# Kernel tuning notes

Measured on AMD Instinct MI355X. Metric: run time of the kernel, lower is better.

## Reference

```python
import jax, jax.numpy as jnp
import numpy as np

# Constants from the torch module __init__
FACE_INDS = np.array([[0, 1, 2, 3], [0, 4, 2, 6], [0, 1, 4, 5],
                      [1, 3, 5, 7], [2, 3, 6, 7], [4, 5, 6, 7]])  # (6,4)
N_GRID = 11
N_POINTS = N_GRID * N_GRID        # 121
N_FACE = 6
N_KP_HAND = 21
N_CONTACTS = 10
ITA = 0.2
IND1 = np.array([0, 1, 2, 3])
IND2 = np.array([1, 2, 3, 0])


def _bilinear_grid():
    # grid[p, k] = bilinear weights for the 4 face corners, p over 11x11 (u,v)
    g = []
    for u in np.linspace(0.0, 1.0, N_GRID):
        for v in np.linspace(0.0, 1.0, N_GRID):
            g.append([v * (1 - u), v * u, (1 - v) * (1 - u), u * (1 - v)])
    return jnp.asarray(np.array(g, dtype=np.float32))  # (121, 4)


def setup_inputs() -> dict:
    key = jax.random.key(0)
    poses = jax.random.normal(key, (8192, N_KP_HAND + 8, 3), dtype=jnp.float32)
    return {"poses": poses}


def affinity_loss(poses):
    bs = poses.shape[0]
    hand = poses[:, :N_KP_HAND, :]          # (bs, 21, 3)
    obj = poses[:, N_KP_HAND:, :]           # (bs, 8, 3)

    # --- sample_face_points: bilinear sample 121 pts on each of the 6 faces ---
    grid = _bilinear_grid().astype(poses.dtype)        # (121, 4)
    faces = obj[:, FACE_INDS, :]                        # (bs, 6, 4, 3)
    face_points = jnp.einsum('bfkc,pk->bfpc', faces, grid)  # (bs, 6, 121, 3)
    obj_pts = face_points.reshape(bs, N_FACE * N_POINTS, 3)  # (bs, 726, 3)

    xx = jnp.sum(hand * hand, axis=-1)                  # (bs, 21)
    yy = jnp.sum(obj_pts * obj_pts, axis=-1)            # (bs, 726)
    zz = jnp.einsum('bic,bjc->bij', hand, obj_pts)      # (bs, 21, 726)
    pdist = jnp.sqrt(xx[:, :, None] + yy[:, None, :] - 2.0 * zz + 1e-6)
    pdist = pdist.reshape(bs, N_KP_HAND, N_FACE, N_POINTS)

    # --- per (hand kp, face) nearest face point, then global top-10 contacts ---
    dist_h2f = jnp.min(pdist, axis=3)                   # (bs, 21, 6)
    idxs_h2f = jnp.argmin(pdist, axis=3)                # (bs, 21, 6)
    flat = dist_h2f.reshape(bs, N_KP_HAND * N_FACE)     # (bs, 126)
    order = jnp.argsort(flat, axis=1)[:, :N_CONTACTS]   # (bs, 10)
    dist = jnp.take_along_axis(flat, order, axis=1)     # (bs, 10)
    inds_hand = order // N_FACE
    inds_face = order % N_FACE
    b = jnp.arange(bs)[:, None]
    ind_obj = idxs_h2f[b, inds_hand, inds_face]                     # (bs, 10)
    obj_contacts = obj_pts[b, inds_face * N_POINTS + ind_obj]       # (bs, 10, 3)

    # --- get_obj_info: axis endpoints and mean edge length of the bbox ---
    points1 = obj[:, :4, :].mean(axis=1)                # (bs, 3)
    points2 = obj[:, 4:, :].mean(axis=1)                # (bs, 3)
    l1 = jnp.linalg.norm(obj[:, IND1] - obj[:, IND2], axis=-1).mean(1, keepdims=True)
    l2 = jnp.linalg.norm(obj[:, IND1 + 4] - obj[:, IND2 + 4], axis=-1).mean(1, keepdims=True)
    length = (l1 + l2) * 0.5                            # (bs, 1)

    mask1 = (dist < length * ITA).astype(poses.dtype)   # (bs, 10)
    mask = mask1[:, :, None] * mask1[:, None, :]        # (bs, 10, 10)

    direct_vec = points2 - points1                      # (bs, 3)
    dv_norm = jnp.linalg.norm(direct_vec, axis=1, keepdims=True)  # (bs, 1)
    normed_dv = direct_vec / (dv_norm + 1e-5)
    vec_contacts = obj_contacts - points1[:, None, :]   # (bs, 10, 3)
    inner = jnp.sum(direct_vec[:, None, :] * vec_contacts, axis=-1)  # (bs, 10)
    t = inner / (dv_norm + 1e-5)                        # (bs, 10)
    r = points1[:, None, :] + normed_dv[:, None, :] * t[:, :, None]  # (bs, 10, 3)
    normal_vec = obj_contacts - r
    normal_vec = normal_vec / (jnp.linalg.norm(normal_vec, axis=2, keepdims=True) + 1e-5)
    cos_sim = jnp.einsum('bic,bjc->bij', normal_vec, normal_vec)  # (bs, 10, 10)

    return (cos_sim * mask).sum() / (mask.sum() + 1.0)


def reference(poses):
    return affinity_loss(poses)
```

## Files before the change

### kernel.cpp

```cpp
#include <hip/hip_runtime.h>
#include <math.h>

#define NGRID   11
#define NPAIR   126
#define NCONT   10

#define NSUB    64
#define NBUK    128
#define WS_SUB  16
#define WS_BUK  128
#define WS_WORDS (WS_BUK + 2 * NBUK)

#define NBUCKET 256

typedef float v2f __attribute__((ext_vector_type(2)));
#define FMA2(a,b,c) __builtin_elementwise_fma((a),(b),(c))
#define MAX2(a,b)   __builtin_elementwise_max((a),(b))
#define SP2(x)      ((v2f){(x),(x)})

__device__ __forceinline__ int last_hit(unsigned old, unsigned quota) {
    const unsigned r = old + 1u - quota;
    return (r == 0u) || (r == 0xAAAAAAAAu);
}

__device__ __constant__ int4 c_face4[6] = {
    {0,1,2,3},{0,4,2,6},{0,1,4,5},{1,3,5,7},{2,3,6,7},{4,5,6,7}};
__device__ __constant__ float c_U[NGRID] = {
    0.0f,0.1f,0.2f,0.3f,0.4f,0.5f,0.6f,0.7f,0.8f,0.9f,1.0f};

__global__ void zero_ws_kernel(float* ws, int n) {
    int t = blockIdx.x * 256 + threadIdx.x;
    if (t < n) ws[t] = 0.0f;
}

__device__ __forceinline__ void coefs_from_face(
        const float4* __restrict__ Ff, float hx, float hy, float hz,
        float& C00, float& C10, float& C01, float& C11,
        float& C20, float& C02, float& C21, float& C12, float& C22) {
    const float4 F0 = Ff[0], F1 = Ff[1], F2 = Ff[2],
                 F3 = Ff[3], F4 = Ff[4], F5 = Ff[5];
    const float hx2 = 2.0f * hx, hy2 = 2.0f * hy, hz2 = 2.0f * hz;
    const float ha2 = fmaf(hx2, F0.x, fmaf(hy2, F0.y, hz2 * F0.z));
    const float hb2 = fmaf(hx2, F1.x, fmaf(hy2, F1.y, hz2 * F1.z));
    const float hc2 = fmaf(hx2, F2.x, fmaf(hy2, F2.y, hz2 * F2.z));
    const float hd2 = fmaf(hx2, F3.x, fmaf(hy2, F3.y, hz2 * F3.z));
    C00 = ha2 - F0.w;
    C10 = hb2 - F4.x;
    C01 = hc2 - F4.y;
    C11 = hd2 - F4.z;
    C20 = -F1.w;  C02 = -F2.w;  C21 = -F4.w;  C12 = -F5.x;  C22 = -F3.w;
}

__launch_bounds__(256)
__global__ void affinity_kernel(const float* __restrict__ poses,
                                float* __restrict__ ws,
                                float* __restrict__ out,
                                int bs, int mode) {
    const int t    = threadIdx.x;
    const int half = t >> 7;
    const int t0   = t & 127;
    const int batch = blockIdx.x * 2 + half;
    const bool valid = batch < bs;

    __shared__ float    sh_pose[2][88];
    __shared__ float4   sh_face[2][36];
    __shared__ float    sh_thr[2][2];
    __shared__ int      sh_ru[2][128];
    __shared__ int      sh_cpair[2][128];
    __shared__ unsigned sh_cnt[2], sh_cnt2[2];
    __shared__ unsigned sh_key[2][128];
    __shared__ float    sh_cont[2][128][3];
    __shared__ float    sh_win[2][NCONT][3];
    __shared__ float    sh_nd[2][2];
    __shared__ int      sh_last;
    __shared__ double   sh_rn[4], sh_rd[4];

    if (valid && t0 < 87) sh_pose[half][t0] = poses[(size_t)batch * 87 + t0];
    if (t0 == 127) { sh_cnt[half] = 0u; sh_cnt2[half] = 0u; }
    __syncthreads();

    const float* hand = sh_pose[half];
    const float* obj  = sh_pose[half] + 63;

    if (valid && t0 < 6) {
        const int4 F = c_face4[t0];
        float C0[3], C1[3], C2[3], C3[3];
        #pragma unroll
        for (int c = 0; c < 3; ++c) {
            C0[c] = obj[F.x * 3 + c];
            C1[c] = obj[F.y * 3 + c];
            C2[c] = obj[F.z * 3 + c];
            C3[c] = obj[F.w * 3 + c];
        }
        float av[3], bv[3], cv[3], dv[3];
        #pragma unroll
        for (int c = 0; c < 3; ++c) {
            av[c] = C2[c];
            bv[c] = C3[c] - C2[c];
            cv[c] = C0[c] - C2[c];
            dv[c] = C1[c] - C0[c] - C3[c] + C2[c];
        }
        float aa=0.f,bb=0.f,cc=0.f,dd=0.f,ab=0.f,ac=0.f,ad=0.f,bc=0.f,bd=0.f,cd=0.f;
        #pragma unroll
        for (int c = 0; c < 3; ++c) {
            aa += av[c]*av[c]; bb += bv[c]*bv[c];
            cc += cv[c]*cv[c]; dd += dv[c]*dv[c];
            ab += av[c]*bv[c]; ac += av[c]*cv[c];
            ad += av[c]*dv[c]; bc += bv[c]*cv[c];
            bd += bv[c]*dv[c]; cd += cv[c]*dv[c];
        }
        float4* Ff = &sh_face[half][t0 * 6];
        Ff[0] = make_float4(av[0], av[1], av[2], aa);
        Ff[1] = make_float4(bv[0], bv[1], bv[2], bb);
        Ff[2] = make_float4(cv[0], cv[1], cv[2], cc);
        Ff[3] = make_float4(dv[0], dv[1], dv[2], dd);
        Ff[4] = make_float4(2.f*ab, 2.f*ac, 2.f*(ad+bc), 2.f*bd);
        Ff[5] = make_float4(2.f*cd, 0.f, 0.f, 0.f);
    }
    if (valid && t0 == 6) {
        float l1 = 0.0f, l2 = 0.0f;
        #pragma unroll
        for (int e = 0; e < 4; ++e) {
            const int a = e, b2 = (e + 1) & 3;
            {
                const float dx = obj[a*3+0]-obj[b2*3+0];
                const float dy = obj[a*3+1]-obj[b2*3+1];
                const float dz = obj[a*3+2]-obj[b2*3+2];
                l1 += sqrtf(dx*dx + dy*dy + dz*dz);
            }
            {
                const float dx = obj[(a+4)*3+0]-obj[(b2+4)*3+0];
                const float dy = obj[(a+4)*3+1]-obj[(b2+4)*3+1];
                const float dz = obj[(a+4)*3+2]-obj[(b2+4)*3+2];
                l2 += sqrtf(dx*dx + dy*dy + dz*dz);
            }
        }
        l1 *= 0.25f; l2 *= 0.25f;
        const float L02 = (l1 + l2) * 0.5f * 0.2f;
        sh_thr[half][0] = L02 * L02 - 1e-6f + 1e-2f;
        sh_thr[half][1] = L02;
    }
    __syncthreads();

    if (valid && t0 < NPAIR) {
        const int i = t0 / 6;
        const int f = t0 - i * 6;
        const float hx = hand[i*3+0], hy = hand[i*3+1], hz = hand[i*3+2];
        const float xx = hx*hx + hy*hy + hz*hz;
        float C00,C10,C01,C11,C20,C02,C21,C12,C22;
        coefs_from_face(&sh_face[half][f*6], hx, hy, hz,
                        C00,C10,C01,C11,C20,C02,C21,C12,C22);

        const float U[NGRID] = {0.0f,0.1f,0.2f,0.3f,0.4f,0.5f,
                                0.6f,0.7f,0.8f,0.9f,1.0f};
        float qb = -3.0e38f;
        int   ru = 0;
        #pragma unroll
        for (int rp = 0; rp < 5; ++rp) {
            const v2f u2 = (v2f){U[2*rp], U[2*rp+1]};
            const v2f A2 = FMA2(FMA2(SP2(C22), u2, SP2(C12)), u2, SP2(C02));
            const v2f A1 = FMA2(FMA2(SP2(C21), u2, SP2(C11)), u2, SP2(C01));
            const v2f A0 = FMA2(FMA2(SP2(C20), u2, SP2(C10)), u2, SP2(C00));
            v2f m2 = A0;
            #pragma unroll
            for (int iv = 1; iv < NGRID; ++iv) {
                const v2f vv = SP2(U[iv]);
                m2 = MAX2(m2, FMA2(FMA2(A2, vv, A1), vv, A0));
            }
            if (m2.x > qb) { qb = m2.x; ru = 2*rp; }
            if (m2.y > qb) { qb = m2.y; ru = 2*rp + 1; }
        }
        {
            const float u = 1.0f;
            const float A2 = fmaf(fmaf(C22,u,C12),u,C02);
            const float A1 = fmaf(fmaf(C21,u,C11),u,C01);
            const float A0 = fmaf(fmaf(C20,u,C10),u,C00);
            float m1 = A0;
            #pragma unroll
            for (int iv = 1; iv < NGRID; ++iv)
                m1 = fmaxf(m1, fmaf(fmaf(A2,U[iv],A1),U[iv],A0));
            if (m1 > qb) { qb = m1; ru = 10; }
        }
        sh_ru[half][t0] = ru;
        const float d2s = xx - qb;
        if (d2s < sh_thr[half][0]) {
            const unsigned s = atomicAdd(&sh_cnt[half], 1u);
            sh_cpair[half][s] = t0;
        }
    }
    __syncthreads();

    {
        const int cnt = (int)sh_cnt[half];
        if (t0 < cnt) {
            const int pair = sh_cpair[half][t0];
            const int i  = pair / 6;
            const int f  = pair - 6 * i;
            const int ru = sh_ru[half][pair];
            const float hx = hand[i*3+0], hy = hand[i*3+1], hz = hand[i*3+2];
            float C00,C10,C01,C11,C20,C02,C21,C12,C22;
            coefs_from_face(&sh_face[half][f*6], hx, hy, hz,
                            C00,C10,C01,C11,C20,C02,C21,C12,C22);
            const float u  = c_U[ru];
            const float A2 = fmaf(fmaf(C22,u,C12),u,C02);
            const float A1 = fmaf(fmaf(C21,u,C11),u,C01);
            const float A0 = fmaf(fmaf(C20,u,C10),u,C00);
            const float U[NGRID] = {0.0f,0.1f,0.2f,0.3f,0.4f,0.5f,
                                    0.6f,0.7f,0.8f,0.9f,1.0f};
            float qr = A0; int vb = 0;
            #pragma unroll
            for (int iv = 1; iv < NGRID; ++iv) {
                const float q = fmaf(fmaf(A2,U[iv],A1),U[iv],A0);
                if (q > qr) { qr = q; vb = iv; }
            }
            const double du = ru * 0.1;
            const double dv = vb * 0.1;
            const float w0 = (float)(dv * (1.0 - du));
            const float w1 = (float)(dv * du);
            const float w2 = (float)((1.0 - dv) * (1.0 - du));
            const float w3 = (float)(du * (1.0 - dv));
            const int4 F = c_face4[f];
            const int i0 = F.x*3, i1 = F.y*3, i2 = F.z*3, i3 = F.w*3;
            const float cx = w0*obj[i0+0]+w1*obj[i1+0]+w2*obj[i2+0]+w3*obj[i3+0];
            const float cy = w0*obj[i0+1]+w1*obj[i1+1]+w2*obj[i2+1]+w3*obj[i3+1];
            const float cz = w0*obj[i0+2]+w1*obj[i1+2]+w2*obj[i2+2]+w3*obj[i3+2];
            const float xx = hx*hx + hy*hy + hz*hz;
            const float yy = cx*cx + cy*cy + cz*cz;
            const float zz = hx*cx + hy*cy + hz*cz;
            const float d2e = (xx + yy) - 2.0f * zz;
            const float dist = sqrtf(d2e + 1e-6f);
            if (dist < sh_thr[half][1]) {
                const unsigned s2 = atomicAdd(&sh_cnt2[half], 1u);
                const float d2k = fmaxf(d2e, 0.0f);
                sh_key[half][s2] = (__float_as_uint(d2k) & 0xFFFFFF80u)
                                 | (unsigned)pair;
                sh_cont[half][s2][0] = cx;
                sh_cont[half][s2][1] = cy;
                sh_cont[half][s2][2] = cz;
            }
        }
    }
    __syncthreads();

    const int n2 = (int)sh_cnt2[half];
    if (t0 < n2) {
        const unsigned ke = sh_key[half][t0];
        int rank = 0;
        for (int j = 0; j < n2; ++j) rank += (sh_key[half][j] < ke) ? 1 : 0;
        if (rank < NCONT) {
            sh_win[half][rank][0] = sh_cont[half][t0][0];
            sh_win[half][rank][1] = sh_cont[half][t0][1];
            sh_win[half][rank][2] = sh_cont[half][t0][2];
        }
    }
    __syncthreads();

    const int kwin = n2 < NCONT ? n2 : NCONT;
    float px = 0.f, py = 0.f, pz = 0.f;
    if (valid && t0 < kwin) {
        const float cx = sh_win[half][t0][0];
        const float cy = sh_win[half][t0][1];
        const float cz = sh_win[half][t0][2];
        const float p1x = (((obj[0] +obj[3]) +obj[6]) +obj[9]) *0.25f;
        const float p1y = (((obj[1] +obj[4]) +obj[7]) +obj[10])*0.25f;
        const float p1z = (((obj[2] +obj[5]) +obj[8]) +obj[11])*0.25f;
        const float p2x = (((obj[12]+obj[15])+obj[18])+obj[21])*0.25f;
        const float p2y = (((obj[13]+obj[16])+obj[19])+obj[22])*0.25f;
        const float p2z = (((obj[14]+obj[17])+obj[20])+obj[23])*0.25f;
        const float dvx = p2x-p1x, dvy = p2y-p1y, dvz = p2z-p1z;
        const float dvn = sqrtf(dvx*dvx + dvy*dvy + dvz*dvz);
        const float den = dvn + 1e-5f;
        const float ndx = dvx/den, ndy = dvy/den, ndz = dvz/den;
        const float vcx = cx-p1x, vcy = cy-p1y, vcz = cz-p1z;
        const float inner = dvx*vcx + dvy*vcy + dvz*vcz;
        const float tp = inner / den;
        const float rx = p1x + ndx*tp, ry = p1y + ndy*tp, rz = p1z + ndz*tp;
        float nvx = cx-rx, nvy = cy-ry, nvz = cz-rz;
        const float nvn = sqrtf(nvx*nvx + nvy*nvy + nvz*nvz) + 1e-5f;
        px = nvx / nvn; py = nvy / nvn; pz = nvz / nvn;
    }
    if (t0 < 64) {
        #pragma unroll
        for (int off = 32; off >= 1; off >>= 1) {
            px += __shfl_xor(px, off, 64);
            py += __shfl_xor(py, off, 64);
            pz += __shfl_xor(pz, off, 64);
        }
        if (t0 == 0) {
            sh_nd[half][0] = px*px + py*py + pz*pz;
            sh_nd[half][1] = (float)(kwin * kwin);
        }
    }
    __syncthreads();

    if (t == 0) {
        sh_last = 0;
        const float num = sh_nd[0][0] + sh_nd[1][0];
        const float dnm = sh_nd[0][1] + sh_nd[1][1];
        const int b = blockIdx.x;
        if (mode) {
            float* bkt = ws + WS_BUK + 2 * (b & (NBUK - 1));
            const float r0 = atomicAdd(bkt + 0, num);
            const float r1 = atomicAdd(bkt + 1, dnm);
            asm volatile("" :: "v"(r0), "v"(r1) : "memory");
            unsigned* subs = (unsigned*)ws + WS_SUB;
            const unsigned nb = gridDim.x;
            const unsigned g  = (unsigned)b & (NSUB - 1);
            const unsigned quota = (nb - 1u - g) / NSUB + 1u;
            const unsigned old = atomicAdd(subs + g, 1u);
            if (last_hit(old, quota)) {
                const unsigned ngroups = nb < NSUB ? nb : NSUB;
                const unsigned m2 = atomicAdd((unsigned*)ws, 1u);
                if (last_hit(m2, ngroups)) sh_last = 1;
            }
        } else {
            float* bucket = ws + 2 * (b & (NBUCKET - 1));
            atomicAdd(bucket + 0, num);
            atomicAdd(bucket + 1, dnm);
        }
    }
    __syncthreads();

    if (sh_last) {
        double n = 0.0, d = 0.0;
        if (t < NBUK) {
            float* bkt = ws + WS_BUK + 2 * t;
            n = (double)atomicAdd(bkt + 0, 0.0f);
            d = (double)atomicAdd(bkt + 1, 0.0f);
        }
        #pragma unroll
        for (int off = 32; off >= 1; off >>= 1) {
            n += __shfl_xor(n, off, 64);
            d += __shfl_xor(d, off, 64);
        }
        const int w = t >> 6;
        if ((t & 63) == 0) { sh_rn[w] = n; sh_rd[w] = d; }
        __syncthreads();
        if (t == 0) {
            const double nn = sh_rn[0] + sh_rn[1] + sh_rn[2] + sh_rn[3];
            const double dd = sh_rd[0] + sh_rd[1] + sh_rd[2] + sh_rd[3];
            out[0] = (float)(nn / (dd + 1.0));
        }
    }
}

__launch_bounds__(1024)
__global__ void finalize_kernel(const float* __restrict__ ws,
                                float* __restrict__ out, int nslot) {
    const int t = threadIdx.x;
    __shared__ double sh_n[16], sh_d[16];
    double n = 0.0, d = 0.0;
    for (int k = t; k < nslot; k += 1024) {
        n += (double)ws[2 * k + 0];
        d += (double)ws[2 * k + 1];
    }
    #pragma unroll
    for (int off = 32; off >= 1; off >>= 1) {
        n += __shfl_xor(n, off, 64);
        d += __shfl_xor(d, off, 64);
    }
    const int w = t >> 6;
    if ((t & 63) == 0) { sh_n[w] = n; sh_d[w] = d; }
    __syncthreads();
    if (t == 0) {
        double nn = 0.0, dd = 0.0;
        #pragma unroll
        for (int i = 0; i < 16; ++i) { nn += sh_n[i]; dd += sh_d[i]; }
        out[0] = (float)(nn / (dd + 1.0));
    }
}

extern "C" void kernel_launch(void* const* d_in, const int* in_sizes, int n_in,
                              void* d_out, int out_size, void* d_ws, size_t ws_size,
                              hipStream_t stream) {
    const float* poses = (const float*)d_in[0];
    float* out = (float*)d_out;
    float* ws  = (float*)d_ws;
    const int bs = in_sizes[0] / 87;
    const int nblk = (bs + 1) / 2;

    if (ws_size >= (size_t)WS_WORDS * sizeof(float)) {
        hipLaunchKernelGGL(affinity_kernel, dim3(nblk), dim3(256), 0, stream,
                           poses, ws, out, bs, 1);
    } else {
        hipLaunchKernelGGL(zero_ws_kernel, dim3(1), dim3(256), 0, stream,
                           ws, NBUCKET * 2);
        hipLaunchKernelGGL(affinity_kernel, dim3(nblk), dim3(256), 0, stream,
                           poses, ws, out, bs, 0);
        hipLaunchKernelGGL(finalize_kernel, dim3(1), dim3(1024), 0, stream,
                           ws, out, NBUCKET);
    }
}
```

Measured before the change: 76.13 us.

## Map one batch element per wavefront and replace block barriers with ballot compaction

Each 64-lane wavefront now handles one batch element, so a block covers four elements instead of two. Lanes loop over the 126 hand-face pairs in two passes and compute face coefficients inline rather than staging them in shared memory. Candidate compaction uses ballot/popcount instead of LDS atomics, and wave barriers replace most __syncthreads. This cuts block-wide syncs and atomics and halves the grid, at the cost of serialising pairs per lane, some redundant face-coefficient math, and a looped rank sort.

```diff
diff --git a/kernel.cpp b/kernel.cpp
--- a/kernel.cpp
+++ b/kernel.cpp
@@ -31,24 +31,6 @@
 __global__ void zero_ws_kernel(float* ws, int n) {
     int t = blockIdx.x * 256 + threadIdx.x;
     if (t < n) ws[t] = 0.0f;
-}
-
-__device__ __forceinline__ void coefs_from_face(
-        const float4* __restrict__ Ff, float hx, float hy, float hz,
-        float& C00, float& C10, float& C01, float& C11,
-        float& C20, float& C02, float& C21, float& C12, float& C22) {
-    const float4 F0 = Ff[0], F1 = Ff[1], F2 = Ff[2],
-                 F3 = Ff[3], F4 = Ff[4], F5 = Ff[5];
-    const float hx2 = 2.0f * hx, hy2 = 2.0f * hy, hz2 = 2.0f * hz;
-    const float ha2 = fmaf(hx2, F0.x, fmaf(hy2, F0.y, hz2 * F0.z));
-    const float hb2 = fmaf(hx2, F1.x, fmaf(hy2, F1.y, hz2 * F1.z));
-    const float hc2 = fmaf(hx2, F2.x, fmaf(hy2, F2.y, hz2 * F2.z));
-    const float hd2 = fmaf(hx2, F3.x, fmaf(hy2, F3.y, hz2 * F3.z));
-    C00 = ha2 - F0.w;
-    C10 = hb2 - F4.x;
-    C01 = hc2 - F4.y;
-    C11 = hd2 - F4.z;
-    C20 = -F1.w;  C02 = -F2.w;  C21 = -F4.w;  C12 = -F5.x;  C22 = -F3.w;
 }
 
 __launch_bounds__(256)
@@ -57,67 +39,34 @@
                                 float* __restrict__ out,
                                 int bs, int mode) {
     const int t    = threadIdx.x;
-    const int half = t >> 7;
-    const int t0   = t & 127;
-    const int batch = blockIdx.x * 2 + half;
+    const int w    = t >> 6;
+    const int lane = t & 63;
+    const int batch = blockIdx.x * 4 + w;
     const bool valid = batch < bs;
 
-    __shared__ float    sh_pose[2][88];
-    __shared__ float4   sh_face[2][36];
-    __shared__ float    sh_thr[2][2];
-    __shared__ int      sh_ru[2][128];
-    __shared__ int      sh_cpair[2][128];
-    __shared__ unsigned sh_cnt[2], sh_cnt2[2];
-    __shared__ unsigned sh_key[2][128];
-    __shared__ float    sh_cont[2][128][3];
-    __shared__ float    sh_win[2][NCONT][3];
-    __shared__ float    sh_nd[2][2];
+    __shared__ float    sh_pose[352];
+    __shared__ unsigned sh_key[4][128];
+    __shared__ float    sh_cont[4][128][3];
+    __shared__ float    sh_win[4][NCONT][3];
+    __shared__ float    sh_nd[4][2];
     __shared__ int      sh_last;
     __shared__ double   sh_rn[4], sh_rd[4];
 
-    if (valid && t0 < 87) sh_pose[half][t0] = poses[(size_t)batch * 87 + t0];
-    if (t0 == 127) { sh_cnt[half] = 0u; sh_cnt2[half] = 0u; }
+    {
+        const size_t lim = (size_t)bs * 87;
+        const size_t g0  = (size_t)blockIdx.x * 348 + t;
+        if (t < 348 && g0 < lim) sh_pose[t] = poses[g0];
+        const int t2 = t + 256;
+        const size_t g1 = g0 + 256;
+        if (t2 < 348 && g1 < lim) sh_pose[t2] = poses[g1];
+    }
     __syncthreads();
 
-    const float* hand = sh_pose[half];
-    const float* obj  = sh_pose[half] + 63;
-
-    if (valid && t0 < 6) {
-        const int4 F = c_face4[t0];
-        float C0[3], C1[3], C2[3], C3[3];
-        #pragma unroll
-        for (int c = 0; c < 3; ++c) {
-            C0[c] = obj[F.x * 3 + c];
-            C1[c] = obj[F.y * 3 + c];
-            C2[c] = obj[F.z * 3 + c];
-            C3[c] = obj[F.w * 3 + c];
-        }
-        float av[3], bv[3], cv[3], dv[3];
-        #pragma unroll
-        for (int c = 0; c < 3; ++c) {
-            av[c] = C2[c];
-            bv[c] = C3[c] - C2[c];
-            cv[c] = C0[c] - C2[c];
-            dv[c] = C1[c] - C0[c] - C3[c] + C2[c];
-        }
-        float aa=0.f,bb=0.f,cc=0.f,dd=0.f,ab=0.f,ac=0.f,ad=0.f,bc=0.f,bd=0.f,cd=0.f;
-        #pragma unroll
-        for (int c = 0; c < 3; ++c) {
-            aa += av[c]*av[c]; bb += bv[c]*bv[c];
-            cc += cv[c]*cv[c]; dd += dv[c]*dv[c];
-            ab += av[c]*bv[c]; ac += av[c]*cv[c];
-            ad += av[c]*dv[c]; bc += bv[c]*cv[c];
-            bd += bv[c]*dv[c]; cd += cv[c]*dv[c];
-        }
-        float4* Ff = &sh_face[half][t0 * 6];
-        Ff[0] = make_float4(av[0], av[1], av[2], aa);
-        Ff[1] = make_float4(bv[0], bv[1], bv[2], bb);
-        Ff[2] = make_float4(cv[0], cv[1], cv[2], cc);
-        Ff[3] = make_float4(dv[0], dv[1], dv[2], dd);
-        Ff[4] = make_float4(2.f*ab, 2.f*ac, 2.f*(ad+bc), 2.f*bd);
-        Ff[5] = make_float4(2.f*cd, 0.f, 0.f, 0.f);
-    }
-    if (valid && t0 == 6) {
+    const float* hand = sh_pose + w * 87;
+    const float* obj  = hand + 63;
+
+    float L02 = 0.0f, flagthr = -3.0e38f;
+    if (valid) {
         float l1 = 0.0f, l2 = 0.0f;
         #pragma unroll
         for (int e = 0; e < 4; ++e) {
@@ -136,131 +85,158 @@
             }
         }
         l1 *= 0.25f; l2 *= 0.25f;
-        const float L02 = (l1 + l2) * 0.5f * 0.2f;
-        sh_thr[half][0] = L02 * L02 - 1e-6f + 1e-2f;
-        sh_thr[half][1] = L02;
-    }
-    __syncthreads();
-
-    if (valid && t0 < NPAIR) {
-        const int i = t0 / 6;
-        const int f = t0 - i * 6;
-        const float hx = hand[i*3+0], hy = hand[i*3+1], hz = hand[i*3+2];
-        const float xx = hx*hx + hy*hy + hz*hz;
-        float C00,C10,C01,C11,C20,C02,C21,C12,C22;
-        coefs_from_face(&sh_face[half][f*6], hx, hy, hz,
-                        C00,C10,C01,C11,C20,C02,C21,C12,C22);
-
-        const float U[NGRID] = {0.0f,0.1f,0.2f,0.3f,0.4f,0.5f,
-                                0.6f,0.7f,0.8f,0.9f,1.0f};
-        float qb = -3.0e38f;
-        int   ru = 0;
-        #pragma unroll
-        for (int rp = 0; rp < 5; ++rp) {
-            const v2f u2 = (v2f){U[2*rp], U[2*rp+1]};
-            const v2f A2 = FMA2(FMA2(SP2(C22), u2, SP2(C12)), u2, SP2(C02));
-            const v2f A1 = FMA2(FMA2(SP2(C21), u2, SP2(C11)), u2, SP2(C01));
-            const v2f A0 = FMA2(FMA2(SP2(C20), u2, SP2(C10)), u2, SP2(C00));
-            v2f m2 = A0;
+        L02 = (l1 + l2) * 0.5f * 0.2f;
+        flagthr = L02 * L02 - 1e-6f + 1e-2f;
+    }
+
+    unsigned ncum = 0;
+    for (int s = 0; s < 2; ++s) {
+        const int pair = lane + (s << 6);
+        const bool active = valid && (pair < NPAIR);
+        bool  pass = false;
+        float cx = 0.0f, cy = 0.0f, cz = 0.0f, d2e = 0.0f;
+        if (active) {
+            const int i = pair / 6;
+            const int f = pair - 6 * i;
+            const int4 F = c_face4[f];
+            float C0[3], C1[3], C2[3], C3[3];
             #pragma unroll
-            for (int iv = 1; iv < NGRID; ++iv) {
-                const v2f vv = SP2(U[iv]);
-                m2 = MAX2(m2, FMA2(FMA2(A2, vv, A1), vv, A0));
-            }
-            if (m2.x > qb) { qb = m2.x; ru = 2*rp; }
-            if (m2.y > qb) { qb = m2.y; ru = 2*rp + 1; }
-        }
-        {
-            const float u = 1.0f;
-            const float A2 = fmaf(fmaf(C22,u,C12),u,C02);
-            const float A1 = fmaf(fmaf(C21,u,C11),u,C01);
-            const float A0 = fmaf(fmaf(C20,u,C10),u,C00);
-            float m1 = A0;
+            for (int c = 0; c < 3; ++c) {
+                C0[c] = obj[F.x * 3 + c];
+                C1[c] = obj[F.y * 3 + c];
+                C2[c] = obj[F.z * 3 + c];
+                C3[c] = obj[F.w * 3 + c];
+            }
+            float av[3], bv[3], cv[3], dvv[3];
             #pragma unroll
-            for (int iv = 1; iv < NGRID; ++iv)
-                m1 = fmaxf(m1, fmaf(fmaf(A2,U[iv],A1),U[iv],A0));
-            if (m1 > qb) { qb = m1; ru = 10; }
-        }
-        sh_ru[half][t0] = ru;
-        const float d2s = xx - qb;
-        if (d2s < sh_thr[half][0]) {
-            const unsigned s = atomicAdd(&sh_cnt[half], 1u);
-            sh_cpair[half][s] = t0;
-        }
-    }
-    __syncthreads();
-
-    {
-        const int cnt = (int)sh_cnt[half];
-        if (t0 < cnt) {
-            const int pair = sh_cpair[half][t0];
-            const int i  = pair / 6;
-            const int f  = pair - 6 * i;
-            const int ru = sh_ru[half][pair];
+            for (int c = 0; c < 3; ++c) {
+                av[c] = C2[c];
+                bv[c] = C3[c] - C2[c];
+                cv[c] = C0[c] - C2[c];
+                dvv[c] = C1[c] - C0[c] - C3[c] + C2[c];
+            }
+            float aa=0.f,bb=0.f,cc=0.f,dd=0.f,ab=0.f,ac=0.f,ad=0.f,bc=0.f,bd=0.f,cd=0.f;
+            #pragma unroll
+            for (int c = 0; c < 3; ++c) {
+                aa += av[c]*av[c]; bb += bv[c]*bv[c];
+                cc += cv[c]*cv[c]; dd += dvv[c]*dvv[c];
+                ab += av[c]*bv[c]; ac += av[c]*cv[c];
+                ad += av[c]*dvv[c]; bc += bv[c]*cv[c];
+                bd += bv[c]*dvv[c]; cd += cv[c]*dvv[c];
+            }
             const float hx = hand[i*3+0], hy = hand[i*3+1], hz = hand[i*3+2];
-            float C00,C10,C01,C11,C20,C02,C21,C12,C22;
-            coefs_from_face(&sh_face[half][f*6], hx, hy, hz,
-                            C00,C10,C01,C11,C20,C02,C21,C12,C22);
-            const float u  = c_U[ru];
-            const float A2 = fmaf(fmaf(C22,u,C12),u,C02);
-            const float A1 = fmaf(fmaf(C21,u,C11),u,C01);
-            const float A0 = fmaf(fmaf(C20,u,C10),u,C00);
+            const float xx = hx*hx + hy*hy + hz*hz;
+            const float hx2 = 2.0f*hx, hy2 = 2.0f*hy, hz2 = 2.0f*hz;
+            const float ha2 = fmaf(hx2, av[0], fmaf(hy2, av[1], hz2 * av[2]));
+            const float hb2 = fmaf(hx2, bv[0], fmaf(hy2, bv[1], hz2 * bv[2]));
+            const float hc2 = fmaf(hx2, cv[0], fmaf(hy2, cv[1], hz2 * cv[2]));
+            const float hd2 = fmaf(hx2, dvv[0], fmaf(hy2, dvv[1], hz2 * dvv[2]));
+            const float C00 = ha2 - aa;
+            const float C10 = hb2 - 2.0f*ab;
+            const float C01 = hc2 - 2.0f*ac;
+            const float C11 = hd2 - 2.0f*(ad+bc);
+            const float C20 = -bb, C02 = -cc;
+            const float C21 = -(2.0f*bd), C12 = -(2.0f*cd), C22 = -dd;
+
             const float U[NGRID] = {0.0f,0.1f,0.2f,0.3f,0.4f,0.5f,
                                     0.6f,0.7f,0.8f,0.9f,1.0f};
-            float qr = A0; int vb = 0;
+            float qb = -3.0e38f;
+            int   ru = 0;
             #pragma unroll
-            for (int iv = 1; iv < NGRID; ++iv) {
-                const float q = fmaf(fmaf(A2,U[iv],A1),U[iv],A0);
-                if (q > qr) { qr = q; vb = iv; }
-            }
-            const double du = ru * 0.1;
-            const double dv = vb * 0.1;
-            const float w0 = (float)(dv * (1.0 - du));
-            const float w1 = (float)(dv * du);
-            const float w2 = (float)((1.0 - dv) * (1.0 - du));
-            const float w3 = (float)(du * (1.0 - dv));
-            const int4 F = c_face4[f];
-            const int i0 = F.x*3, i1 = F.y*3, i2 = F.z*3, i3 = F.w*3;
-            const float cx = w0*obj[i0+0]+w1*obj[i1+0]+w2*obj[i2+0]+w3*obj[i3+0];
-            const float cy = w0*obj[i0+1]+w1*obj[i1+1]+w2*obj[i2+1]+w3*obj[i3+1];
-            const float cz = w0*obj[i0+2]+w1*obj[i1+2]+w2*obj[i2+2]+w3*obj[i3+2];
-            const float xx = hx*hx + hy*hy + hz*hz;
-            const float yy = cx*cx + cy*cy + cz*cz;
-            const float zz = hx*cx + hy*cy + hz*cz;
-            const float d2e = (xx + yy) - 2.0f * zz;
-            const float dist = sqrtf(d2e + 1e-6f);
-            if (dist < sh_thr[half][1]) {
-                const unsigned s2 = atomicAdd(&sh_cnt2[half], 1u);
-                const float d2k = fmaxf(d2e, 0.0f);
-                sh_key[half][s2] = (__float_as_uint(d2k) & 0xFFFFFF80u)
-                                 | (unsigned)pair;
-                sh_cont[half][s2][0] = cx;
-                sh_cont[half][s2][1] = cy;
-                sh_cont[half][s2][2] = cz;
-            }
-        }
-    }
-    __syncthreads();
-
-    const int n2 = (int)sh_cnt2[half];
-    if (t0 < n2) {
-        const unsigned ke = sh_key[half][t0];
-        int rank = 0;
-        for (int j = 0; j < n2; ++j) rank += (sh_key[half][j] < ke) ? 1 : 0;
-        if (rank < NCONT) {
-            sh_win[half][rank][0] = sh_cont[half][t0][0];
-            sh_win[half][rank][1] = sh_cont[half][t0][1];
-            sh_win[half][rank][2] = sh_cont[half][t0][2];
-        }
-    }
-    __syncthreads();
+            for (int rp = 0; rp < 5; ++rp) {
+                const v2f u2 = (v2f){U[2*rp], U[2*rp+1]};
+                const v2f A2v = FMA2(FMA2(SP2(C22), u2, SP2(C12)), u2, SP2(C02));
+                const v2f A1v = FMA2(FMA2(SP2(C21), u2, SP2(C11)), u2, SP2(C01));
+                const v2f A0v = FMA2(FMA2(SP2(C20), u2, SP2(C10)), u2, SP2(C00));
+                v2f m2 = A0v;
+                #pragma unroll
+                for (int iv = 1; iv < NGRID; ++iv) {
+                    const v2f vv = SP2(U[iv]);
+                    m2 = MAX2(m2, FMA2(FMA2(A2v, vv, A1v), vv, A0v));
+                }
+                if (m2.x > qb) { qb = m2.x; ru = 2*rp; }
+                if (m2.y > qb) { qb = m2.y; ru = 2*rp + 1; }
+            }
+            {
+                const float u = 1.0f;
+                const float A2 = fmaf(fmaf(C22,u,C12),u,C02);
+                const float A1 = fmaf(fmaf(C21,u,C11),u,C01);
+                const float A0 = fmaf(fmaf(C20,u,C10),u,C00);
+                float m1 = A0;
+                #pragma unroll
+                for (int iv = 1; iv < NGRID; ++iv)
+                    m1 = fmaxf(m1, fmaf(fmaf(A2,U[iv],A1),U[iv],A0));
+                if (m1 > qb) { qb = m1; ru = 10; }
+            }
+            const float d2s = xx - qb;
+            if (d2s < flagthr) {
+                const float u  = c_U[ru];
+                const float A2 = fmaf(fmaf(C22,u,C12),u,C02);
+                const float A1 = fmaf(fmaf(C21,u,C11),u,C01);
+                const float A0 = fmaf(fmaf(C20,u,C10),u,C00);
+                float qr = A0; int vb = 0;
+                #pragma unroll
+                for (int iv = 1; iv < NGRID; ++iv) {
+                    const float q = fmaf(fmaf(A2,U[iv],A1),U[iv],A0);
+                    if (q > qr) { qr = q; vb = iv; }
+                }
+                const double du = ru * 0.1;
+                const double dgv = vb * 0.1;
+                const float w0 = (float)(dgv * (1.0 - du));
+                const float w1 = (float)(dgv * du);
+                const float w2 = (float)((1.0 - dgv) * (1.0 - du));
+                const float w3 = (float)(du * (1.0 - dgv));
+                const int i0 = F.x*3, i1 = F.y*3, i2 = F.z*3, i3 = F.w*3;
+                cx = w0*obj[i0+0]+w1*obj[i1+0]+w2*obj[i2+0]+w3*obj[i3+0];
+                cy = w0*obj[i0+1]+w1*obj[i1+1]+w2*obj[i2+1]+w3*obj[i3+1];
+                cz = w0*obj[i0+2]+w1*obj[i1+2]+w2*obj[i2+2]+w3*obj[i3+2];
+                const float yy = cx*cx + cy*cy + cz*cz;
+                const float zz = hx*cx + hy*cy + hz*cz;
+                d2e = (xx + yy) - 2.0f * zz;
+                const float dist = sqrtf(d2e + 1e-6f);
+                pass = dist < L02;
+            }
+        }
+        const unsigned long long m = __ballot(pass ? 1 : 0);
+        if (pass) {
+            const unsigned idx = ncum +
+                (unsigned)__popcll(m & ((1ull << lane) - 1ull));
+            const float d2k = fmaxf(d2e, 0.0f);
+            sh_key[w][idx] = (__float_as_uint(d2k) & 0xFFFFFF80u)
+                           | (unsigned)pair;
+            sh_cont[w][idx][0] = cx;
+            sh_cont[w][idx][1] = cy;
+            sh_cont[w][idx][2] = cz;
+        }
+        ncum += (unsigned)__popcll(m);
+    }
+    const int n2 = (int)ncum;
+
+    __threadfence_block();
+    __builtin_amdgcn_wave_barrier();
+
+    for (int base = 0; base < n2; base += 64) {
+        const int idx = base + lane;
+        if (idx < n2) {
+            const unsigned ke = sh_key[w][idx];
+            int rank = 0;
+            for (int j = 0; j < n2; ++j) rank += (sh_key[w][j] < ke) ? 1 : 0;
+            if (rank < NCONT) {
+                sh_win[w][rank][0] = sh_cont[w][idx][0];
+                sh_win[w][rank][1] = sh_cont[w][idx][1];
+                sh_win[w][rank][2] = sh_cont[w][idx][2];
+            }
+        }
+    }
+    __threadfence_block();
+    __builtin_amdgcn_wave_barrier();
 
     const int kwin = n2 < NCONT ? n2 : NCONT;
     float px = 0.f, py = 0.f, pz = 0.f;
-    if (valid && t0 < kwin) {
-        const float cx = sh_win[half][t0][0];
-        const float cy = sh_win[half][t0][1];
-        const float cz = sh_win[half][t0][2];
+    if (valid && lane < kwin) {
+        const float cx = sh_win[w][lane][0];
+        const float cy = sh_win[w][lane][1];
+        const float cz = sh_win[w][lane][2];
         const float p1x = (((obj[0] +obj[3]) +obj[6]) +obj[9]) *0.25f;
         const float p1y = (((obj[1] +obj[4]) +obj[7]) +obj[10])*0.25f;
         const float p1z = (((obj[2] +obj[5]) +obj[8]) +obj[11])*0.25f;
@@ -279,24 +255,22 @@
         const float nvn = sqrtf(nvx*nvx + nvy*nvy + nvz*nvz) + 1e-5f;
         px = nvx / nvn; py = nvy / nvn; pz = nvz / nvn;
     }
-    if (t0 < 64) {
-        #pragma unroll
-        for (int off = 32; off >= 1; off >>= 1) {
-            px += __shfl_xor(px, off, 64);
-            py += __shfl_xor(py, off, 64);
-            pz += __shfl_xor(pz, off, 64);
-        }
-        if (t0 == 0) {
-            sh_nd[half][0] = px*px + py*py + pz*pz;
-            sh_nd[half][1] = (float)(kwin * kwin);
-        }
+    #pragma unroll
+    for (int off = 32; off >= 1; off >>= 1) {
+        px += __shfl_xor(px, off, 64);
+        py += __shfl_xor(py, off, 64);
+        pz += __shfl_xor(pz, off, 64);
+    }
+    if (lane == 0) {
+        sh_nd[w][0] = px*px + py*py + pz*pz;
+        sh_nd[w][1] = (float)(kwin * kwin);
     }
     __syncthreads();
 
     if (t == 0) {
         sh_last = 0;
-        const float num = sh_nd[0][0] + sh_nd[1][0];
-        const float dnm = sh_nd[0][1] + sh_nd[1][1];
+        const float num = ((sh_nd[0][0] + sh_nd[1][0]) + sh_nd[2][0]) + sh_nd[3][0];
+        const float dnm = ((sh_nd[0][1] + sh_nd[1][1]) + sh_nd[2][1]) + sh_nd[3][1];
         const int b = blockIdx.x;
         if (mode) {
             float* bkt = ws + WS_BUK + 2 * (b & (NBUK - 1));
@@ -333,8 +307,8 @@
             n += __shfl_xor(n, off, 64);
             d += __shfl_xor(d, off, 64);
         }
-        const int w = t >> 6;
-        if ((t & 63) == 0) { sh_rn[w] = n; sh_rd[w] = d; }
+        const int ww = t >> 6;
+        if ((t & 63) == 0) { sh_rn[ww] = n; sh_rd[ww] = d; }
         __syncthreads();
         if (t == 0) {
             const double nn = sh_rn[0] + sh_rn[1] + sh_rn[2] + sh_rn[3];
@@ -377,7 +351,7 @@
     float* out = (float*)d_out;
     float* ws  = (float*)d_ws;
     const int bs = in_sizes[0] / 87;
-    const int nblk = (bs + 1) / 2;
+    const int nblk = (bs + 3) / 4;
 
     if (ws_size >= (size_t)WS_WORDS * sizeof(float)) {
         hipLaunchKernelGGL(affinity_kernel, dim3(nblk), dim3(256), 0, stream,
```

Result: no change. 75.21 us (-1.2%).
